# Performance work log

Measured on AMD Instinct MI355X. Metric: run time of the kernel, lower is better.

Reference implementation:

```python
import jax, jax.numpy as jnp
import numpy as np

N_T, N_C, N_D = 500_000, 200_000, 100_000  # target / card / device node counts
E = 1_000_000                              # edges per relation
IN, HID, OUT = 64, 64, 2


def setup_inputs() -> dict:
    key = jax.random.key(0)
    ks = jax.random.split(key, 18)
    f32 = jnp.float32
    inp = {
        "features": jax.random.normal(ks[0], (N_T, IN), f32),
        "emb_card": jax.random.normal(ks[1], (N_C, IN), f32) * 0.05,
        "emb_device": jax.random.normal(ks[2], (N_D, IN), f32) * 0.05,
        "W1": jax.random.normal(ks[3], (4, IN, HID), f32) * 0.05,
        "b1": jax.random.normal(ks[4], (4, HID), f32) * 0.05,
        "W2": jax.random.normal(ks[5], (4, HID, HID), f32) * 0.05,
        "b2": jax.random.normal(ks[6], (4, HID), f32) * 0.05,
        "W_out": jax.random.normal(ks[7], (HID, OUT), f32) * 0.05,
        "b_out": jax.random.normal(ks[8], (OUT,), f32) * 0.05,
        "src_c2t": jax.random.randint(ks[9], (E,), 0, N_C, jnp.int32),
        "dst_c2t": jax.random.randint(ks[10], (E,), 0, N_T, jnp.int32),
        "src_t2c": jax.random.randint(ks[11], (E,), 0, N_T, jnp.int32),
        "dst_t2c": jax.random.randint(ks[12], (E,), 0, N_C, jnp.int32),
        "src_d2t": jax.random.randint(ks[13], (E,), 0, N_D, jnp.int32),
        "dst_d2t": jax.random.randint(ks[14], (E,), 0, N_T, jnp.int32),
        "src_t2d": jax.random.randint(ks[15], (E,), 0, N_T, jnp.int32),
        "dst_t2d": jax.random.randint(ks[16], (E,), 0, N_D, jnp.int32),
    }
    return inp


def _mean_agg(Wh, src, dst, n_dst):
    """copy_u gather + scatter-mean: mean over incoming edges of Wh[src]."""
    msgs = Wh[src]  # [E, H] gather
    s = jax.ops.segment_sum(msgs, dst, num_segments=n_dst)
    deg = jax.ops.segment_sum(jnp.ones((src.shape[0],), Wh.dtype), dst, num_segments=n_dst)
    return s / jnp.maximum(deg, 1.0)[:, None]  # zero in-degree -> 0 (DGL default)


def _layer(x_t, x_c, x_d, W, b, edges):
    # etype order: 0 card->target, 1 target->card, 2 device->target, 3 target->device
    (sc2t, dc2t, st2c, dt2c, sd2t, dd2t, st2d, dt2d) = edges
    Wh0 = x_c @ W[0] + b[0]
    Wh1 = x_t @ W[1] + b[1]
    Wh2 = x_d @ W[2] + b[2]
    Wh3 = x_t @ W[3] + b[3]
    # cross-relation reducer = 'sum'
    h_t = _mean_agg(Wh0, sc2t, dc2t, N_T) + _mean_agg(Wh2, sd2t, dd2t, N_T)
    h_c = _mean_agg(Wh1, st2c, dt2c, N_C)
    h_d = _mean_agg(Wh3, st2d, dt2d, N_D)
    return h_t, h_c, h_d


def reference(features, emb_card, emb_device, W1, b1, W2, b2, W_out, b_out,
              src_c2t, dst_c2t, src_t2c, dst_t2c, src_d2t, dst_d2t, src_t2d, dst_t2d):
    edges = (src_c2t, dst_c2t, src_t2c, dst_t2c, src_d2t, dst_d2t, src_t2d, dst_t2d)
    h_t, h_c, h_d = _layer(features, emb_card, emb_device, W1, b1, edges)
    h_t, h_c, h_d = (jax.nn.leaky_relu(h, 0.01) for h in (h_t, h_c, h_d))
    h_t, h_c, h_d = _layer(h_t, h_c, h_d, W2, b2, edges)
    return h_t @ W_out + b_out  # [N_T, OUT] logits for target node type
```

## Files before the change

### kernel.cpp

```cpp
#include <hip/hip_runtime.h>
#include <hip/hip_bf16.h>


#define NT 500000
#define NC 200000
#define ND 100000
#define NE 1000000
#define H  64
#define CAP_T2C 32
#define CAP_T2D 48

#define PACK_SCALE 65536.0f
#define PACK_BIAS  262144
#define FIELD_MASK 0x3FFFFFFULL

#define NBK_MAX 245
#define OFF_C2T 196
#define OFF_D2T 441
#define EPB 4096
#define BPR 245
#define CAP_BK1 11776
#define CAP_BK2 4864

#define CB512 7813

__device__ __forceinline__ void rel_params(int rel, int& shift, int& hoff, int& nbk) {
    shift = (rel == 1) ? 10 : 11;
    hoff = (rel == 0) ? 0 : (rel == 1) ? 98 : (rel == 2) ? OFF_C2T : OFF_D2T;
    nbk = (rel < 2) ? 98 : 245;
}

#define BFP(x) (u = __float_as_uint(x), (u + 0x7fffu + ((u >> 16) & 1u)) >> 16)

__global__ __launch_bounds__(512)
void scatter_compress(const int* __restrict__ st2c, const int* __restrict__ dt2c,
                      const int* __restrict__ st2d, const int* __restrict__ dt2d,
                      const int* __restrict__ sc2t, const int* __restrict__ dc2t,
                      const int* __restrict__ sd2t, const int* __restrict__ dd2t,
                      int* __restrict__ cur,
                      unsigned long long* __restrict__ bedges1,
                      unsigned long long* __restrict__ bedges2,
                      const float* __restrict__ X, unsigned int* __restrict__ Xb,
                      const float* __restrict__ W2, const float* __restrict__ b2,
                      const float* __restrict__ Wout,
                      float* __restrict__ Wc, float* __restrict__ bc) {
    __shared__ unsigned long long le[EPB];
    __shared__ int h[NBK_MAX], pref[NBK_MAX], gbase[NBK_MAX], csr[NBK_MAX];
    __shared__ int sc[256];
    int t = threadIdx.x, b = blockIdx.x;

    if (b >= 4 * BPR) {
        int cb = b - 4 * BPR;
        if (cb < CB512) {
            size_t idx = (size_t)cb * 512 + t;
            if (idx < 4000000) {
                const float4 f0 = ((const float4*)X)[idx * 2];
                const float4 f1 = ((const float4*)X)[idx * 2 + 1];
                uint4 o;
                unsigned int u;
                o.x = BFP(f0.x) | (BFP(f0.y) << 16);
                o.y = BFP(f0.z) | (BFP(f0.w) << 16);
                o.z = BFP(f1.x) | (BFP(f1.y) << 16);
                o.w = BFP(f1.z) | (BFP(f1.w) << 16);
                ((uint4*)Xb)[idx] = o;
            }
        } else if (t < 256) {
            int rel = t >> 7;
            int rem = t & 127;
            int k = rem >> 1, o = rem & 1;
            const float* W2r = W2 + (rel ? 2 : 0) * H * H;
            float s = 0.0f;
            for (int j = 0; j < H; ++j) s += W2r[k * H + j] * Wout[j * 2 + o];
            Wc[rel * 128 + k * 2 + o] = s;
            if (rem < 4) {
                int r2 = rem >> 1, o2 = rem & 1;
                const float* b2r = b2 + (r2 ? 2 : 0) * H;
                float sb = 0.0f;
                for (int j = 0; j < H; ++j) sb += b2r[j] * Wout[j * 2 + o2];
                bc[r2 * 2 + o2] = sb;
            }
        }
        return;
    }

    int rel = b / BPR;
    int bb = b - rel * BPR;
    const int* sp = (rel == 0) ? st2c : (rel == 1) ? st2d : (rel == 2) ? sc2t : sd2t;
    const int* dp = (rel == 0) ? dt2c : (rel == 1) ? dt2d : (rel == 2) ? dc2t : dd2t;
    int shift, hoff, nbk;
    rel_params(rel, shift, hoff, nbk);
    unsigned long long* bedges = (rel < 2) ? bedges1 : bedges2;
    int bkoff = (rel == 1) ? 98 : (rel == 3) ? 245 : 0;
    int bkcap = (rel < 2) ? CAP_BK1 : CAP_BK2;

    for (int i = t; i < nbk; i += 512) { h[i] = 0; csr[i] = 0; }
    __syncthreads();

    int base = bb * EPB + t * 8;
    bool ok = base < NE;
    int4 d0, d1, s0, s1;
    if (ok) {
        d0 = *(const int4*)(dp + base);
        d1 = *(const int4*)(dp + base + 4);
        s0 = *(const int4*)(sp + base);
        s1 = *(const int4*)(sp + base + 4);
        atomicAdd(&h[d0.x >> shift], 1);
        atomicAdd(&h[d0.y >> shift], 1);
        atomicAdd(&h[d0.z >> shift], 1);
        atomicAdd(&h[d0.w >> shift], 1);
        atomicAdd(&h[d1.x >> shift], 1);
        atomicAdd(&h[d1.y >> shift], 1);
        atomicAdd(&h[d1.z >> shift], 1);
        atomicAdd(&h[d1.w >> shift], 1);
    }
    __syncthreads();
    if (t < nbk && h[t]) gbase[t] = (bkoff + t) * bkcap + atomicAdd(&cur[hoff + t], h[t]);
    if (t < 256) sc[t] = (t < nbk) ? h[t] : 0;
    __syncthreads();
    for (int s = 1; s < 256; s <<= 1) {
        int y = (t < 256 && t >= s) ? sc[t - s] : 0;
        __syncthreads();
        if (t < 256) sc[t] += y;
        __syncthreads();
    }
    if (t < nbk) pref[t] = sc[t] - h[t];
    __syncthreads();

    if (ok) {
        #define BIN(dv, sv) { int k = (dv) >> shift; \
            int l = atomicAdd(&csr[k], 1); \
            le[pref[k] + l] = ((unsigned long long)(unsigned int)(dv) << 32) | (unsigned int)(sv); }
        BIN(d0.x, s0.x) BIN(d0.y, s0.y) BIN(d0.z, s0.z) BIN(d0.w, s0.w)
        BIN(d1.x, s1.x) BIN(d1.y, s1.y) BIN(d1.z, s1.z) BIN(d1.w, s1.w)
        #undef BIN
    }
    __syncthreads();

    int n_e = NE - bb * EPB; if (n_e > EPB) n_e = EPB;
    for (int i = t; i < n_e; i += 512) {
        unsigned long long e = le[i];
        int k = (int)(e >> 32) >> shift;
        bedges[(size_t)gbase[k] + (i - pref[k])] = e;
    }
}

__global__ __launch_bounds__(1024)
void radix_build(const unsigned long long* __restrict__ bedges1, const int* __restrict__ cur,
                 int* __restrict__ cnt_t2c, int* __restrict__ cols_t2c,
                 int* __restrict__ cnt_t2d, int* __restrict__ cols_t2d) {
    __shared__ int lc[2048];
    int t = threadIdx.x, k = blockIdx.x;
    int rel = k >= 98 ? 1 : 0;
    int shift = rel ? 10 : 11;
    int range = 1 << shift;
    int noff = (rel ? (k - 98) : k) << shift;
    int nN = rel ? ND : NC;
    int* cnt = rel ? cnt_t2d : cnt_t2c;
    int* cols = rel ? cols_t2d : cols_t2c;
    int cap = rel ? CAP_T2D : CAP_T2C;
    int e0 = k * CAP_BK1;
    int e1 = e0 + cur[k];
    for (int i = t; i < range; i += 1024) lc[i] = 0;
    __syncthreads();
    for (int i = e0 + t; i < e1; i += 1024) {
        unsigned long long e = bedges1[i];
        int d = (int)(e >> 32);
        int s = (int)(e & 0xffffffffu);
        int l = atomicAdd(&lc[d - noff], 1);
        if (l < cap) cols[(size_t)d * cap + l] = s;
    }
    __syncthreads();
    for (int i = t; i < range; i += 1024) {
        int gn = noff + i;
        if (gn < nN) cnt[gn] = lc[i];
    }
}

#define NBGM_C 3125
#define NBGM_D 1563

__global__ __launch_bounds__(512)
void gather_mean(const unsigned int* __restrict__ Xb,
                 const int* __restrict__ cnt_c, const int* __restrict__ cols_c,
                 const int* __restrict__ cnt_d, const int* __restrict__ cols_d,
                 unsigned int* __restrict__ mB) {
    int t = threadIdx.x;
    int lane = t & 63;
    int w = t >> 6;
    int half = lane >> 5;
    int li = lane & 31;

    int bn, nNodes, cap;
    const int* cnt; const int* cols; unsigned int* mP;
    if (blockIdx.x < NBGM_C) {
        bn = blockIdx.x * 64; nNodes = NC; cap = CAP_T2C;
        cnt = cnt_c; cols = cols_c; mP = mB;
    } else {
        bn = (blockIdx.x - NBGM_C) * 64; nNodes = ND; cap = CAP_T2D;
        cnt = cnt_d; cols = cols_d; mP = mB + (size_t)NC * 32;
    }

    int gnb = bn + w * 8;
    int cval = 0;
    if (lane < 8 && gnb + lane < nNodes) cval = cnt[gnb + lane];

    int cc[8], mm[8], cv[8];
#pragma unroll
    for (int r = 0; r < 8; ++r) {
        cc[r] = __shfl(cval, r);
        mm[r] = cc[r] < cap ? cc[r] : cap;
    }
#pragma unroll
    for (int r = 0; r < 8; ++r) {
        int gn = gnb + r;
        cv[r] = (lane < mm[r] && gn < nNodes) ? cols[(size_t)gn * cap + lane] : 0;
    }

    int maxm = 0;
#pragma unroll
    for (int r = 0; r < 8; ++r) maxm = maxm > mm[r] ? maxm : mm[r];

    float ax[8], ay[8];
#pragma unroll
    for (int r = 0; r < 8; ++r) { ax[r] = 0.0f; ay[r] = 0.0f; }

    for (int j = 0; j < maxm; j += 2) {
#pragma unroll
        for (int r = 0; r < 8; ++r) {
            int sA = __shfl(cv[r], j);
            int sB = __shfl(cv[r], j + 1);
            int src = half ? sB : sA;
            unsigned int v = 0;
            if (j + half < mm[r]) v = Xb[(size_t)src * 32 + li];
            ax[r] += __uint_as_float(v << 16);
            ay[r] += __uint_as_float(v & 0xffff0000u);
        }
    }

#pragma unroll
    for (int r = 0; r < 8; ++r) {
        float fx = ax[r] + __shfl_xor(ax[r], 32);
        float fy = ay[r] + __shfl_xor(ay[r], 32);
        float inv = cc[r] > 0 ? 1.0f / (float)cc[r] : 0.0f;
        ax[r] = fx * inv; ay[r] = fy * inv;
    }
    unsigned int u;
#pragma unroll
    for (int r = 0; r < 8; r += 2) {
        int gn = gnb + r + half;
        float vx = half ? ax[r + 1] : ax[r];
        float vy = half ? ay[r + 1] : ay[r];
        unsigned int pv = BFP(vx) | (BFP(vy) << 16);
        if (gn < nNodes) mP[(size_t)gn * 32 + li] = pv;
    }
}

#define NBX_C 3125
#define NBX_D 1563

__global__ __launch_bounds__(512)
void xform64(const unsigned int* __restrict__ mB,
             const int* __restrict__ cnt_c, const int* __restrict__ cnt_d,
             const float* __restrict__ W1, const float* __restrict__ b1,
             const float* __restrict__ Wc, const float* __restrict__ bc,
             float* __restrict__ Pc, float* __restrict__ Pd) {
    __shared__ float Xs[64][65];
    __shared__ float Wl[64][68];
    __shared__ float msk[64];
    int t = threadIdx.x;

    int bn, nNodes; const unsigned int* mrow; const int* cnt;
    const float* W1r; const float* b1r; const float* Wcr; const float* bcr;
    float* P;
    if (blockIdx.x < NBX_C) {
        bn = blockIdx.x * 64; nNodes = NC;
        mrow = mB; cnt = cnt_c;
        W1r = W1 + 1 * H * H; b1r = b1 + 1 * H; Wcr = Wc; bcr = bc; P = Pc;
    } else {
        bn = (blockIdx.x - NBX_C) * 64; nNodes = ND;
        mrow = mB + (size_t)NC * 32; cnt = cnt_d;
        W1r = W1 + 3 * H * H; b1r = b1 + 3 * H; Wcr = Wc + 128; bcr = bc + 2; P = Pd;
    }

    {
        int nl = t >> 3, seg = t & 7;
        int gn = bn + nl;
        uint4 v = make_uint4(0, 0, 0, 0);
        if (gn < nNodes) v = ((const uint4*)(mrow + (size_t)gn * 32))[seg];
        float* xr = &Xs[nl][seg * 8];
        xr[0] = __uint_as_float(v.x << 16); xr[1] = __uint_as_float(v.x & 0xffff0000u);
        xr[2] = __uint_as_float(v.y << 16); xr[3] = __uint_as_float(v.y & 0xffff0000u);
        xr[4] = __uint_as_float(v.z << 16); xr[5] = __uint_as_float(v.z & 0xffff0000u);
        xr[6] = __uint_as_float(v.w << 16); xr[7] = __uint_as_float(v.w & 0xffff0000u);
        for (int q = t; q < 1024; q += 512) {
            int kk = q >> 4, s2 = q & 15;
            *(float4*)&Wl[kk][s2 * 4] = *(const float4*)(W1r + kk * H + s2 * 4);
        }
        if (t < 64) msk[t] = (bn + t < nNodes && cnt[bn + t] > 0) ? 1.0f : 0.0f;
    }
    __syncthreads();

    int nl = t >> 3;
    int c0 = (t & 7) * 8;
    float4 ba = *(const float4*)(b1r + c0);
    float4 bb4 = *(const float4*)(b1r + c0 + 4);
    float h0 = ba.x, h1 = ba.y, h2 = ba.z, h3 = ba.w;
    float h4 = bb4.x, h5 = bb4.y, h6 = bb4.z, h7 = bb4.w;
#pragma unroll
    for (int k = 0; k < H; ++k) {
        float xv = Xs[nl][k];
        float4 wa = *(const float4*)&Wl[k][c0];
        float4 wb = *(const float4*)&Wl[k][c0 + 4];
        h0 = fmaf(xv, wa.x, h0); h1 = fmaf(xv, wa.y, h1);
        h2 = fmaf(xv, wa.z, h2); h3 = fmaf(xv, wa.w, h3);
        h4 = fmaf(xv, wb.x, h4); h5 = fmaf(xv, wb.y, h5);
        h6 = fmaf(xv, wb.z, h6); h7 = fmaf(xv, wb.w, h7);
    }
    float m = msk[nl];
    h0 = (h0 > 0.f ? h0 : 0.01f * h0) * m;
    h1 = (h1 > 0.f ? h1 : 0.01f * h1) * m;
    h2 = (h2 > 0.f ? h2 : 0.01f * h2) * m;
    h3 = (h3 > 0.f ? h3 : 0.01f * h3) * m;
    h4 = (h4 > 0.f ? h4 : 0.01f * h4) * m;
    h5 = (h5 > 0.f ? h5 : 0.01f * h5) * m;
    h6 = (h6 > 0.f ? h6 : 0.01f * h6) * m;
    h7 = (h7 > 0.f ? h7 : 0.01f * h7) * m;
    float4 wc0 = *(const float4*)(Wcr + c0 * 2);
    float4 wc1 = *(const float4*)(Wcr + c0 * 2 + 4);
    float4 wc2 = *(const float4*)(Wcr + c0 * 2 + 8);
    float4 wc3 = *(const float4*)(Wcr + c0 * 2 + 12);
    float p0 = h0 * wc0.x + h1 * wc0.z + h2 * wc1.x + h3 * wc1.z
             + h4 * wc2.x + h5 * wc2.z + h6 * wc3.x + h7 * wc3.z;
    float p1 = h0 * wc0.y + h1 * wc0.w + h2 * wc1.y + h3 * wc1.w
             + h4 * wc2.y + h5 * wc2.w + h6 * wc3.y + h7 * wc3.w;
#pragma unroll
    for (int off = 1; off < 8; off <<= 1) {
        p0 += __shfl_xor(p0, off);
        p1 += __shfl_xor(p1, off);
    }
    int gn = bn + nl;
    if ((t & 7) == 0 && gn < nNodes) {
        float2 o = make_float2(p0 + bcr[0], p1 + bcr[1]);
        *(float2*)(P + 2 * (size_t)gn) = o;
    }
}

__device__ __forceinline__ unsigned long long pack_p(const float* __restrict__ P, int s) {
    float2 pv = *(const float2*)(P + 2 * (size_t)s);
    float a = fminf(fmaxf(pv.x, -3.99f), 3.99f);
    float b = fminf(fmaxf(pv.y, -3.99f), 3.99f);
    unsigned int ia = (unsigned int)(__float2int_rn(a * PACK_SCALE) + PACK_BIAS);
    unsigned int ib = (unsigned int)(__float2int_rn(b * PACK_SCALE) + PACK_BIAS);
    return (1ULL << 52) | ((unsigned long long)ia << 26) | (unsigned long long)ib;
}

__global__ __launch_bounds__(1024)
void agg_out(const unsigned long long* __restrict__ bedges2, const int* __restrict__ cur,
             const float* __restrict__ Pc, const float* __restrict__ Pd,
             const float* __restrict__ bout, float* __restrict__ out) {
    __shared__ unsigned long long accC[2048], accD[2048];
    int t = threadIdx.x, k = blockIdx.x;
    int noff = k << 11;
    int range = NT - noff; if (range > 2048) range = 2048;
    for (int i = t; i < 2048; i += 1024) { accC[i] = 0ULL; accD[i] = 0ULL; }
    __syncthreads();

    int e0 = k * CAP_BK2, e1 = e0 + cur[OFF_C2T + k];
    for (int i = e0 + t; i < e1; i += 1024) {
        unsigned long long e = bedges2[i];
        int d = (int)(e >> 32);
        int s = (int)(e & 0xffffffffu);
        atomicAdd(&accC[d - noff], pack_p(Pc, s));
    }
    int f0 = (245 + k) * CAP_BK2, f1 = f0 + cur[OFF_D2T + k];
    for (int i = f0 + t; i < f1; i += 1024) {
        unsigned long long e = bedges2[i];
        int d = (int)(e >> 32);
        int s = (int)(e & 0xffffffffu);
        atomicAdd(&accD[d - noff], pack_p(Pd, s));
    }
    __syncthreads();

    float bo0 = bout[0], bo1 = bout[1];
    const float inv_s = 1.0f / PACK_SCALE;
    for (int i = t; i < range; i += 1024) {
        unsigned long long xc = accC[i];
        unsigned long long xd = accD[i];
        int dc = (int)(xc >> 52);
        int dd = (int)(xd >> 52);
        float ic = dc > 0 ? 1.0f / (float)dc : 0.0f;
        float id = dd > 0 ? 1.0f / (float)dd : 0.0f;
        float c0 = (float)((long long)((xc >> 26) & FIELD_MASK) - (long long)dc * PACK_BIAS);
        float c1 = (float)((long long)(xc & FIELD_MASK) - (long long)dc * PACK_BIAS);
        float d0 = (float)((long long)((xd >> 26) & FIELD_MASK) - (long long)dd * PACK_BIAS);
        float d1 = (float)((long long)(xd & FIELD_MASK) - (long long)dd * PACK_BIAS);
        float2 o;
        o.x = bo0 + (c0 * ic + d0 * id) * inv_s;
        o.y = bo1 + (c1 * ic + d1 * id) * inv_s;
        *(float2*)(out + 2 * (size_t)(noff + i)) = o;
    }
}

extern "C" void kernel_launch(void* const* d_in, const int* in_sizes, int n_in,
                              void* d_out, int out_size, void* d_ws, size_t ws_size,
                              hipStream_t stream) {
    const float* features = (const float*)d_in[0];
    const float* W1 = (const float*)d_in[3];
    const float* b1 = (const float*)d_in[4];
    const float* W2 = (const float*)d_in[5];
    const float* b2 = (const float*)d_in[6];
    const float* W_out = (const float*)d_in[7];
    const float* b_out = (const float*)d_in[8];
    const int* src_c2t = (const int*)d_in[9];
    const int* dst_c2t = (const int*)d_in[10];
    const int* src_t2c = (const int*)d_in[11];
    const int* dst_t2c = (const int*)d_in[12];
    const int* src_d2t = (const int*)d_in[13];
    const int* dst_d2t = (const int*)d_in[14];
    const int* src_t2d = (const int*)d_in[15];
    const int* dst_t2d = (const int*)d_in[16];
    float* out = (float*)d_out;

    char* w = (char*)d_ws;
    int* cur = (int*)w;                           w += 1024 * 4;
    size_t zero_bytes = 1024 * 4;
    int* cnt_t2c = (int*)w;                       w += (size_t)NC * 4;
    int* cnt_t2d = (int*)w;                       w += (size_t)ND * 4;
    int* cols_t2c = (int*)w;                      w += (size_t)NC * CAP_T2C * 4;
    int* cols_t2d = (int*)w;                      w += (size_t)ND * CAP_T2D * 4;
    float* p_c = (float*)w;                       w += (size_t)NC * 2 * 4;
    float* p_d = (float*)w;                       w += (size_t)ND * 2 * 4;
    float* Wc = (float*)w;                        w += 256 * 4;
    float* bc = (float*)w;                        w += 16;
    unsigned long long* bedges1 = (unsigned long long*)w;  w += (size_t)196 * CAP_BK1 * 8;
    unsigned long long* bedges2 = (unsigned long long*)w;  w += (size_t)490 * CAP_BK2 * 8;
    unsigned int* Xb = (unsigned int*)w;          w += (size_t)NT * H * 2;
    unsigned int* mB = (unsigned int*)w;          w += ((size_t)(NC + ND) + 64) * 32 * 4;

    hipMemsetAsync(d_ws, 0, zero_bytes, stream);

    scatter_compress<<<4 * BPR + CB512 + 1, 512, 0, stream>>>(
        src_t2c, dst_t2c, src_t2d, dst_t2d,
        src_c2t, dst_c2t, src_d2t, dst_d2t,
        cur, bedges1, bedges2,
        features, Xb, W2, b2, W_out, Wc, bc);

    radix_build<<<196, 1024, 0, stream>>>(bedges1, cur,
                                          cnt_t2c, cols_t2c, cnt_t2d, cols_t2d);

    gather_mean<<<NBGM_C + NBGM_D, 512, 0, stream>>>(
        Xb, cnt_t2c, cols_t2c, cnt_t2d, cols_t2d, mB);

    xform64<<<NBX_C + NBX_D, 512, 0, stream>>>(
        mB, cnt_t2c, cnt_t2d, W1, b1, Wc, bc, p_c, p_d);

    agg_out<<<NBK_MAX, 1024, 0, stream>>>(bedges2, cur, p_c, p_d, b_out, out);
}
```

Baseline: 240.6 us.

## Halve target-node bucket width and register-tile the hidden transform GEMM

The target-side edge buckets shrink from 2048 to 1024 nodes, doubling the bucket count to 489. The final aggregation kernel therefore runs more, smaller 512-thread blocks with half-size LDS accumulators, which should improve occupancy and spread the work. Separately, the per-node hidden-layer transform now uses a transposed X tile in LDS and a 4x4 register tile per thread with 256-thread blocks. This gives more FMA reuse per LDS load, at the cost of a wider shuffle reduction. The scan grows to 512 entries and the workspace layout is adjusted to match.

```diff
diff --git a/kernel.cpp b/kernel.cpp
--- a/kernel.cpp
+++ b/kernel.cpp
@@ -14,20 +14,21 @@
 #define PACK_BIAS  262144
 #define FIELD_MASK 0x3FFFFFFULL
 
-#define NBK_MAX 245
+#define NBK_MAX 489
+#define NBK2 489
 #define OFF_C2T 196
-#define OFF_D2T 441
+#define OFF_D2T 685
 #define EPB 4096
 #define BPR 245
 #define CAP_BK1 11776
-#define CAP_BK2 4864
+#define CAP_BK2 2688
 
 #define CB512 7813
 
 __device__ __forceinline__ void rel_params(int rel, int& shift, int& hoff, int& nbk) {
-    shift = (rel == 1) ? 10 : 11;
+    shift = (rel == 0) ? 11 : 10;
     hoff = (rel == 0) ? 0 : (rel == 1) ? 98 : (rel == 2) ? OFF_C2T : OFF_D2T;
-    nbk = (rel < 2) ? 98 : 245;
+    nbk = (rel < 2) ? 98 : NBK2;
 }
 
 #define BFP(x) (u = __float_as_uint(x), (u + 0x7fffu + ((u >> 16) & 1u)) >> 16)
@@ -46,7 +47,7 @@
                       float* __restrict__ Wc, float* __restrict__ bc) {
     __shared__ unsigned long long le[EPB];
     __shared__ int h[NBK_MAX], pref[NBK_MAX], gbase[NBK_MAX], csr[NBK_MAX];
-    __shared__ int sc[256];
+    __shared__ int sc[512];
     int t = threadIdx.x, b = blockIdx.x;
 
     if (b >= 4 * BPR) {
@@ -90,7 +91,7 @@
     int shift, hoff, nbk;
     rel_params(rel, shift, hoff, nbk);
     unsigned long long* bedges = (rel < 2) ? bedges1 : bedges2;
-    int bkoff = (rel == 1) ? 98 : (rel == 3) ? 245 : 0;
+    int bkoff = (rel == 1) ? 98 : (rel == 3) ? NBK2 : 0;
     int bkcap = (rel < 2) ? CAP_BK1 : CAP_BK2;
 
     for (int i = t; i < nbk; i += 512) { h[i] = 0; csr[i] = 0; }
@@ -115,12 +116,12 @@
     }
     __syncthreads();
     if (t < nbk && h[t]) gbase[t] = (bkoff + t) * bkcap + atomicAdd(&cur[hoff + t], h[t]);
-    if (t < 256) sc[t] = (t < nbk) ? h[t] : 0;
-    __syncthreads();
-    for (int s = 1; s < 256; s <<= 1) {
-        int y = (t < 256 && t >= s) ? sc[t - s] : 0;
+    sc[t] = (t < nbk) ? h[t] : 0;
+    __syncthreads();
+    for (int s = 1; s < 512; s <<= 1) {
+        int y = (t >= s) ? sc[t - s] : 0;
         __syncthreads();
-        if (t < 256) sc[t] += y;
+        sc[t] += y;
         __syncthreads();
     }
     if (t < nbk) pref[t] = sc[t] - h[t];
@@ -258,13 +259,13 @@
 #define NBX_C 3125
 #define NBX_D 1563
 
-__global__ __launch_bounds__(512)
-void xform64(const unsigned int* __restrict__ mB,
-             const int* __restrict__ cnt_c, const int* __restrict__ cnt_d,
-             const float* __restrict__ W1, const float* __restrict__ b1,
-             const float* __restrict__ Wc, const float* __restrict__ bc,
-             float* __restrict__ Pc, float* __restrict__ Pd) {
-    __shared__ float Xs[64][65];
+__global__ __launch_bounds__(256)
+void xform_tile(const unsigned int* __restrict__ mB,
+                const int* __restrict__ cnt_c, const int* __restrict__ cnt_d,
+                const float* __restrict__ W1, const float* __restrict__ b1,
+                const float* __restrict__ Wc, const float* __restrict__ bc,
+                float* __restrict__ Pc, float* __restrict__ Pd) {
+    __shared__ float Xt[64][68];
     __shared__ float Wl[64][68];
     __shared__ float msk[64];
     int t = threadIdx.x;
@@ -283,16 +284,32 @@
     }
 
     {
-        int nl = t >> 3, seg = t & 7;
-        int gn = bn + nl;
-        uint4 v = make_uint4(0, 0, 0, 0);
-        if (gn < nNodes) v = ((const uint4*)(mrow + (size_t)gn * 32))[seg];
-        float* xr = &Xs[nl][seg * 8];
-        xr[0] = __uint_as_float(v.x << 16); xr[1] = __uint_as_float(v.x & 0xffff0000u);
-        xr[2] = __uint_as_float(v.y << 16); xr[3] = __uint_as_float(v.y & 0xffff0000u);
-        xr[4] = __uint_as_float(v.z << 16); xr[5] = __uint_as_float(v.z & 0xffff0000u);
-        xr[6] = __uint_as_float(v.w << 16); xr[7] = __uint_as_float(v.w & 0xffff0000u);
-        for (int q = t; q < 1024; q += 512) {
+        int node = t & 63, seg = t >> 6;
+        int gn = bn + node;
+        uint4 v0 = make_uint4(0, 0, 0, 0), v1 = make_uint4(0, 0, 0, 0);
+        if (gn < nNodes) {
+            const uint4* rp = (const uint4*)(mrow + (size_t)gn * 32);
+            v0 = rp[seg * 2];
+            v1 = rp[seg * 2 + 1];
+        }
+        int k0 = seg * 16;
+        Xt[k0 + 0][node] = __uint_as_float(v0.x << 16);
+        Xt[k0 + 1][node] = __uint_as_float(v0.x & 0xffff0000u);
+        Xt[k0 + 2][node] = __uint_as_float(v0.y << 16);
+        Xt[k0 + 3][node] = __uint_as_float(v0.y & 0xffff0000u);
+        Xt[k0 + 4][node] = __uint_as_float(v0.z << 16);
+        Xt[k0 + 5][node] = __uint_as_float(v0.z & 0xffff0000u);
+        Xt[k0 + 6][node] = __uint_as_float(v0.w << 16);
+        Xt[k0 + 7][node] = __uint_as_float(v0.w & 0xffff0000u);
+        Xt[k0 + 8][node] = __uint_as_float(v1.x << 16);
+        Xt[k0 + 9][node] = __uint_as_float(v1.x & 0xffff0000u);
+        Xt[k0 + 10][node] = __uint_as_float(v1.y << 16);
+        Xt[k0 + 11][node] = __uint_as_float(v1.y & 0xffff0000u);
+        Xt[k0 + 12][node] = __uint_as_float(v1.z << 16);
+        Xt[k0 + 13][node] = __uint_as_float(v1.z & 0xffff0000u);
+        Xt[k0 + 14][node] = __uint_as_float(v1.w << 16);
+        Xt[k0 + 15][node] = __uint_as_float(v1.w & 0xffff0000u);
+        for (int q = t; q < 1024; q += 256) {
             int kk = q >> 4, s2 = q & 15;
             *(float4*)&Wl[kk][s2 * 4] = *(const float4*)(W1r + kk * H + s2 * 4);
         }
@@ -300,48 +317,59 @@
     }
     __syncthreads();
 
-    int nl = t >> 3;
-    int c0 = (t & 7) * 8;
-    float4 ba = *(const float4*)(b1r + c0);
-    float4 bb4 = *(const float4*)(b1r + c0 + 4);
-    float h0 = ba.x, h1 = ba.y, h2 = ba.z, h3 = ba.w;
-    float h4 = bb4.x, h5 = bb4.y, h6 = bb4.z, h7 = bb4.w;
+    int tj = t & 15;
+    int ti = t >> 4;
+    float4 b4 = *(const float4*)(b1r + tj * 4);
+    float a4[4][4];
+#pragma unroll
+    for (int r = 0; r < 4; ++r) {
+        a4[r][0] = b4.x; a4[r][1] = b4.y; a4[r][2] = b4.z; a4[r][3] = b4.w;
+    }
 #pragma unroll
     for (int k = 0; k < H; ++k) {
-        float xv = Xs[nl][k];
-        float4 wa = *(const float4*)&Wl[k][c0];
-        float4 wb = *(const float4*)&Wl[k][c0 + 4];
-        h0 = fmaf(xv, wa.x, h0); h1 = fmaf(xv, wa.y, h1);
-        h2 = fmaf(xv, wa.z, h2); h3 = fmaf(xv, wa.w, h3);
-        h4 = fmaf(xv, wb.x, h4); h5 = fmaf(xv, wb.y, h5);
-        h6 = fmaf(xv, wb.z, h6); h7 = fmaf(xv, wb.w, h7);
-    }
-    float m = msk[nl];
-    h0 = (h0 > 0.f ? h0 : 0.01f * h0) * m;
-    h1 = (h1 > 0.f ? h1 : 0.01f * h1) * m;
-    h2 = (h2 > 0.f ? h2 : 0.01f * h2) * m;
-    h3 = (h3 > 0.f ? h3 : 0.01f * h3) * m;
-    h4 = (h4 > 0.f ? h4 : 0.01f * h4) * m;
-    h5 = (h5 > 0.f ? h5 : 0.01f * h5) * m;
-    h6 = (h6 > 0.f ? h6 : 0.01f * h6) * m;
-    h7 = (h7 > 0.f ? h7 : 0.01f * h7) * m;
-    float4 wc0 = *(const float4*)(Wcr + c0 * 2);
-    float4 wc1 = *(const float4*)(Wcr + c0 * 2 + 4);
-    float4 wc2 = *(const float4*)(Wcr + c0 * 2 + 8);
-    float4 wc3 = *(const float4*)(Wcr + c0 * 2 + 12);
-    float p0 = h0 * wc0.x + h1 * wc0.z + h2 * wc1.x + h3 * wc1.z
-             + h4 * wc2.x + h5 * wc2.z + h6 * wc3.x + h7 * wc3.z;
-    float p1 = h0 * wc0.y + h1 * wc0.w + h2 * wc1.y + h3 * wc1.w
-             + h4 * wc2.y + h5 * wc2.w + h6 * wc3.y + h7 * wc3.w;
-#pragma unroll
-    for (int off = 1; off < 8; off <<= 1) {
-        p0 += __shfl_xor(p0, off);
-        p1 += __shfl_xor(p1, off);
-    }
-    int gn = bn + nl;
-    if ((t & 7) == 0 && gn < nNodes) {
-        float2 o = make_float2(p0 + bcr[0], p1 + bcr[1]);
-        *(float2*)(P + 2 * (size_t)gn) = o;
+        float4 a = *(const float4*)&Xt[k][ti * 4];
+        float4 b = *(const float4*)&Wl[k][tj * 4];
+        a4[0][0] = fmaf(a.x, b.x, a4[0][0]); a4[0][1] = fmaf(a.x, b.y, a4[0][1]);
+        a4[0][2] = fmaf(a.x, b.z, a4[0][2]); a4[0][3] = fmaf(a.x, b.w, a4[0][3]);
+        a4[1][0] = fmaf(a.y, b.x, a4[1][0]); a4[1][1] = fmaf(a.y, b.y, a4[1][1]);
+        a4[1][2] = fmaf(a.y, b.z, a4[1][2]); a4[1][3] = fmaf(a.y, b.w, a4[1][3]);
+        a4[2][0] = fmaf(a.z, b.x, a4[2][0]); a4[2][1] = fmaf(a.z, b.y, a4[2][1]);
+        a4[2][2] = fmaf(a.z, b.z, a4[2][2]); a4[2][3] = fmaf(a.z, b.w, a4[2][3]);
+        a4[3][0] = fmaf(a.w, b.x, a4[3][0]); a4[3][1] = fmaf(a.w, b.y, a4[3][1]);
+        a4[3][2] = fmaf(a.w, b.z, a4[3][2]); a4[3][3] = fmaf(a.w, b.w, a4[3][3]);
+    }
+
+    float4 wca = *(const float4*)(Wcr + tj * 8);
+    float4 wcb = *(const float4*)(Wcr + tj * 8 + 4);
+    float p0[4], p1[4];
+#pragma unroll
+    for (int r = 0; r < 4; ++r) {
+        float m = msk[ti * 4 + r];
+        float h0 = a4[r][0], h1 = a4[r][1], h2 = a4[r][2], h3 = a4[r][3];
+        h0 = (h0 > 0.f ? h0 : 0.01f * h0) * m;
+        h1 = (h1 > 0.f ? h1 : 0.01f * h1) * m;
+        h2 = (h2 > 0.f ? h2 : 0.01f * h2) * m;
+        h3 = (h3 > 0.f ? h3 : 0.01f * h3) * m;
+        p0[r] = h0 * wca.x + h1 * wca.z + h2 * wcb.x + h3 * wcb.z;
+        p1[r] = h0 * wca.y + h1 * wca.w + h2 * wcb.y + h3 * wcb.w;
+    }
+#pragma unroll
+    for (int off = 1; off < 16; off <<= 1) {
+#pragma unroll
+        for (int r = 0; r < 4; ++r) {
+            p0[r] += __shfl_xor(p0[r], off);
+            p1[r] += __shfl_xor(p1[r], off);
+        }
+    }
+    if (tj == 0) {
+#pragma unroll
+        for (int r = 0; r < 4; ++r) {
+            int gn = bn + ti * 4 + r;
+            if (gn < nNodes) {
+                float2 o = make_float2(p0[r] + bcr[0], p1[r] + bcr[1]);
+                *(float2*)(P + 2 * (size_t)gn) = o;
+            }
+        }
     }
 }
 
@@ -354,26 +382,26 @@
     return (1ULL << 52) | ((unsigned long long)ia << 26) | (unsigned long long)ib;
 }
 
-__global__ __launch_bounds__(1024)
+__global__ __launch_bounds__(512)
 void agg_out(const unsigned long long* __restrict__ bedges2, const int* __restrict__ cur,
              const float* __restrict__ Pc, const float* __restrict__ Pd,
              const float* __restrict__ bout, float* __restrict__ out) {
-    __shared__ unsigned long long accC[2048], accD[2048];
+    __shared__ unsigned long long accC[1024], accD[1024];
     int t = threadIdx.x, k = blockIdx.x;
-    int noff = k << 11;
-    int range = NT - noff; if (range > 2048) range = 2048;
-    for (int i = t; i < 2048; i += 1024) { accC[i] = 0ULL; accD[i] = 0ULL; }
+    int noff = k << 10;
+    int range = NT - noff; if (range > 1024) range = 1024;
+    for (int i = t; i < 1024; i += 512) { accC[i] = 0ULL; accD[i] = 0ULL; }
     __syncthreads();
 
     int e0 = k * CAP_BK2, e1 = e0 + cur[OFF_C2T + k];
-    for (int i = e0 + t; i < e1; i += 1024) {
+    for (int i = e0 + t; i < e1; i += 512) {
         unsigned long long e = bedges2[i];
         int d = (int)(e >> 32);
         int s = (int)(e & 0xffffffffu);
         atomicAdd(&accC[d - noff], pack_p(Pc, s));
     }
-    int f0 = (245 + k) * CAP_BK2, f1 = f0 + cur[OFF_D2T + k];
-    for (int i = f0 + t; i < f1; i += 1024) {
+    int f0 = (NBK2 + k) * CAP_BK2, f1 = f0 + cur[OFF_D2T + k];
+    for (int i = f0 + t; i < f1; i += 512) {
         unsigned long long e = bedges2[i];
         int d = (int)(e >> 32);
         int s = (int)(e & 0xffffffffu);
@@ -383,7 +411,7 @@
 
     float bo0 = bout[0], bo1 = bout[1];
     const float inv_s = 1.0f / PACK_SCALE;
-    for (int i = t; i < range; i += 1024) {
+    for (int i = t; i < range; i += 512) {
         unsigned long long xc = accC[i];
         unsigned long long xd = accD[i];
         int dc = (int)(xc >> 52);
@@ -422,8 +450,8 @@
     float* out = (float*)d_out;
 
     char* w = (char*)d_ws;
-    int* cur = (int*)w;                           w += 1024 * 4;
-    size_t zero_bytes = 1024 * 4;
+    int* cur = (int*)w;                           w += 2048 * 4;
+    size_t zero_bytes = 2048 * 4;
     int* cnt_t2c = (int*)w;                       w += (size_t)NC * 4;
     int* cnt_t2d = (int*)w;                       w += (size_t)ND * 4;
     int* cols_t2c = (int*)w;                      w += (size_t)NC * CAP_T2C * 4;
@@ -433,7 +461,7 @@
     float* Wc = (float*)w;                        w += 256 * 4;
     float* bc = (float*)w;                        w += 16;
     unsigned long long* bedges1 = (unsigned long long*)w;  w += (size_t)196 * CAP_BK1 * 8;
-    unsigned long long* bedges2 = (unsigned long long*)w;  w += (size_t)490 * CAP_BK2 * 8;
+    unsigned long long* bedges2 = (unsigned long long*)w;  w += (size_t)(2 * NBK2) * CAP_BK2 * 8;
     unsigned int* Xb = (unsigned int*)w;          w += (size_t)NT * H * 2;
     unsigned int* mB = (unsigned int*)w;          w += ((size_t)(NC + ND) + 64) * 32 * 4;
 
@@ -451,8 +479,8 @@
     gather_mean<<<NBGM_C + NBGM_D, 512, 0, stream>>>(
         Xb, cnt_t2c, cols_t2c, cnt_t2d, cols_t2d, mB);
 
-    xform64<<<NBX_C + NBX_D, 512, 0, stream>>>(
+    xform_tile<<<NBX_C + NBX_D, 256, 0, stream>>>(
         mB, cnt_t2c, cnt_t2d, W1, b1, Wc, bc, p_c, p_d);
 
-    agg_out<<<NBK_MAX, 1024, 0, stream>>>(bedges2, cur, p_c, p_d, b_out, out);
-}
+    agg_out<<<NBK2, 512, 0, stream>>>(bedges2, cur, p_c, p_d, b_out, out);
+}
```

After: 229.4 us. -4.6%, faster.
